# Kernel optimization log

Measured on AMD Instinct MI355X. Metric: run time of the kernel, lower is better.

The kernel has to match this reference:

```python
import jax, jax.numpy as jnp
import numpy as np

NUM_GROUPS = 32
EPS = 1e-5


def setup_inputs() -> dict:
    key = jax.random.key(0)
    ks = jax.random.split(key, 6)
    B, C, H, W = 8, 128, 64, 64
    d = C // 8
    x = jax.random.normal(ks[0], (B, C, H, W), dtype=jnp.float32)
    # conv 1x1 weights stored as [out_ch, in_ch]; scaled like torch kaiming-uniform-ish
    s = 1.0 / np.sqrt(C)
    return {
        "x": x,
        "gn_w": jnp.ones((C,), jnp.float32),
        "gn_b": jnp.zeros((C,), jnp.float32),
        "q_w": jax.random.normal(ks[1], (d, C), jnp.float32) * s,
        "q_b": jnp.zeros((d,), jnp.float32),
        "k_w": jax.random.normal(ks[2], (d, C), jnp.float32) * s,
        "k_b": jnp.zeros((d,), jnp.float32),
        "v_w": jax.random.normal(ks[3], (C, C), jnp.float32) * s,
        "v_b": jnp.zeros((C,), jnp.float32),
        "p_w": jax.random.normal(ks[4], (C, C), jnp.float32) * s,
        "p_b": jnp.zeros((C,), jnp.float32),
    }


def _group_norm(x, w, b):
    B, C, H, W = x.shape
    g = NUM_GROUPS
    xr = x.reshape(B, g, C // g, H, W)
    mu = xr.mean(axis=(2, 3, 4), keepdims=True)
    var = xr.var(axis=(2, 3, 4), keepdims=True)
    xn = ((xr - mu) * jax.lax.rsqrt(var + EPS)).reshape(B, C, H, W)
    return xn * w[None, :, None, None] + b[None, :, None, None]


def reference(x, gn_w, gn_b, q_w, q_b, k_w, k_b, v_w, v_b, p_w, p_b):
    B, C, H, W = x.shape
    N = H * W
    h_ = _group_norm(x, gn_w, gn_b)            # [B,C,H,W]
    hf = h_.reshape(B, C, N)                   # flatten spatial
    # 1x1 convs == channel matmuls
    q = jnp.einsum('dc,bcn->bnd', q_w, hf) + q_b[None, None, :]   # [B,N,d]
    k = jnp.einsum('dc,bcn->bnd', k_w, hf) + k_b[None, None, :]   # [B,N,d]
    v = jnp.einsum('ec,bcn->ben', v_w, hf) + v_b[None, :, None]   # [B,C,N]
    d = q.shape[-1]
    scale = jnp.asarray(int(d) ** (-0.5), x.dtype)
    attn = jnp.einsum('bid,bjd->bij', q, k) * scale               # [B,N,N]
    attn = jax.nn.softmax(attn, axis=-1)
    a = jnp.einsum('bcj,bij->bci', v, attn)                       # [B,C,N]
    proj = jnp.einsum('ec,bcn->ben', p_w, a) + p_b[None, :, None]
    return x + proj.reshape(B, C, H, W)
```

## Files before the change

kernel.cpp:

```cpp
#include <hip/hip_runtime.h>
#include <math.h>


typedef short v8s __attribute__((ext_vector_type(8)));
typedef float v16f __attribute__((ext_vector_type(16)));

__device__ __forceinline__ unsigned short f2bf_rne(float f) {
  unsigned u = __float_as_uint(f);
  u += 0x7fffu + ((u >> 16) & 1u);
  return (unsigned short)(u >> 16);
}

__device__ __forceinline__ v8s mk8(unsigned a, unsigned b, unsigned c, unsigned d) {
  union { unsigned u[4]; v8s s; } x;
  x.u[0] = a; x.u[1] = b; x.u[2] = c; x.u[3] = d;
  return x.s;
}

__device__ __forceinline__ unsigned pack_trunc(float hi, float lo) {
  return __builtin_amdgcn_perm(__float_as_uint(hi), __float_as_uint(lo), 0x07060302u);
}

#define VT(b, n, c) (((((size_t)(b) * 256 + ((n) >> 4)) << 7) + (c)) * 16 + ((n) & 15))

#define WSB_MURS   0u
#define WSB_WCATB  4096u
#define WSB_BCAT   49152u
#define WSB_PWB    65536u
#define WSB_QBF    131072u
#define WSB_KBF    1310720u
#define WSB_VBF    2621440u

__global__ __launch_bounds__(512)
void gnprep_kernel(const float* __restrict__ x, float* __restrict__ mu_rs,
                   const float* __restrict__ qw, const float* __restrict__ qb,
                   const float* __restrict__ kw, const float* __restrict__ kb,
                   const float* __restrict__ vw, const float* __restrict__ vb,
                   const float* __restrict__ pw,
                   unsigned short* __restrict__ wcatb, float* __restrict__ bcat,
                   unsigned short* __restrict__ pwb) {
  const int id = blockIdx.x;
  {
    const float qs = 0.36067376022224085f;
    int idx = id * 512 + threadIdx.x;
    if (idx < 160 * 128) {
      int o = idx >> 7, c = idx & 127;
      float val;
      if (o < 16)       val = qw[o * 128 + c] * qs;
      else if (o < 32)  val = kw[(o - 16) * 128 + c];
      else              val = vw[(o - 32) * 128 + c];
      wcatb[idx] = f2bf_rne(val);
    } else if (idx < 160 * 128 + 160) {
      int o = idx - 160 * 128;
      bcat[o] = (o < 16) ? qb[o] * qs : (o < 32) ? kb[o - 16] : vb[o - 32];
    } else if (idx < 160 * 128 + 160 + 128 * 128) {
      int j = idx - (160 * 128 + 160);
      pwb[j] = f2bf_rne(pw[j]);
    }
  }
  const int bg = (id & 7) * 32 + (id >> 3);
  const float4* xp = (const float4*)(x + (size_t)bg * 16384);
  float s = 0.f, ss = 0.f;
#pragma unroll
  for (int u = 0; u < 8; ++u) {
    int i = threadIdx.x + u * 512;
    float4 v = xp[i];
    s  += v.x + v.y + v.z + v.w;
    ss += v.x * v.x + v.y * v.y + v.z * v.z + v.w * v.w;
  }
  for (int off = 32; off > 0; off >>= 1) {
    s  += __shfl_down(s, off, 64);
    ss += __shfl_down(ss, off, 64);
  }
  __shared__ float red[16];
  int lane = threadIdx.x & 63, wid = threadIdx.x >> 6;
  if (lane == 0) { red[wid * 2] = s; red[wid * 2 + 1] = ss; }
  __syncthreads();
  if (threadIdx.x == 0) {
    float S = 0.f, SS = 0.f;
    for (int w = 0; w < 8; ++w) { S += red[w * 2]; SS += red[w * 2 + 1]; }
    float mu  = S * (1.0f / 16384.0f);
    float var = SS * (1.0f / 16384.0f) - mu * mu;
    float rs  = rsqrtf(var + 1e-5f);
    mu_rs[bg * 2]     = mu;
    mu_rs[bg * 2 + 1] = rs;
  }
}

#define HS 136

__global__ __launch_bounds__(512)
void qkv_kernel(const float* __restrict__ x, const float* __restrict__ gnw,
                const float* __restrict__ gnb, const float* __restrict__ mu_rs,
                const unsigned short* __restrict__ wcatb, const float* __restrict__ bcat,
                unsigned short* __restrict__ qTb, unsigned short* __restrict__ kbf,
                unsigned short* __restrict__ vbf) {
  __shared__ alignas(16) unsigned short hs[64 * HS];
  __shared__ float scsh[128], shsh[128], bsh[160];
  const int id = blockIdx.x;
  const int b = id & 7, nb = (id >> 3) << 6;
  const int t = threadIdx.x;
  const int w = t >> 6, lane = t & 63, h = lane >> 5, l = lane & 31;
  const int nsub = w & 1, og = w >> 1;

  if (t < 128) {
    float mu = mu_rs[(b * 32 + (t >> 2)) * 2];
    float rs = mu_rs[(b * 32 + (t >> 2)) * 2 + 1];
    float gw = gnw[t], gb = gnb[t];
    scsh[t] = rs * gw; shsh[t] = gb - mu * rs * gw;
  }
  if (t < 160) bsh[t] = bcat[t];
  __syncthreads();

  const int sn = t & 63;
  const int c00 = (t >> 6) * 4;
  const float* xb = x + ((size_t)b * 128 << 12) + nb + sn;
#pragma unroll
  for (int it = 0; it < 4; ++it) {
    const int c0 = c00 + it * 32;
    float f0 = xb[(size_t)(c0)     << 12] * scsh[c0]     + shsh[c0];
    float f1 = xb[(size_t)(c0 + 1) << 12] * scsh[c0 + 1] + shsh[c0 + 1];
    float f2 = xb[(size_t)(c0 + 2) << 12] * scsh[c0 + 2] + shsh[c0 + 2];
    float f3 = xb[(size_t)(c0 + 3) << 12] * scsh[c0 + 3] + shsh[c0 + 3];
    uint2 u;
    u.x = (unsigned)f2bf_rne(f0) | ((unsigned)f2bf_rne(f1) << 16);
    u.y = (unsigned)f2bf_rne(f2) | ((unsigned)f2bf_rne(f3) << 16);
    *(uint2*)(&hs[sn * HS + c0]) = u;
  }
  __syncthreads();

  const int n = nb + nsub * 32 + l;
  const int otbase = (og == 0) ? 0 : og + 1;
  v16f acc[2];
#pragma unroll
  for (int a2 = 0; a2 < 2; ++a2)
#pragma unroll
    for (int r = 0; r < 16; ++r) acc[a2][r] = 0.f;

#pragma unroll
  for (int ks = 0; ks < 8; ++ks) {
    v8s bf = *(const v8s*)(&hs[(nsub * 32 + l) * HS + ks * 16 + 8 * h]);
    {
      v8s af = *(const v8s*)(wcatb + (otbase * 32 + l) * 128 + ks * 16 + 8 * h);
      acc[0] = __builtin_amdgcn_mfma_f32_32x32x16_bf16(af, bf, acc[0], 0, 0, 0);
    }
    if (og == 0) {
      v8s af = *(const v8s*)(wcatb + (32 + l) * 128 + ks * 16 + 8 * h);
      acc[1] = __builtin_amdgcn_mfma_f32_32x32x16_bf16(af, bf, acc[1], 0, 0, 0);
    }
  }

  if (og == 0) {
    const size_t nqk = ((size_t)b * 4096 + n) << 4;
#pragma unroll
    for (int r = 0; r < 16; ++r) {
      int o = 4 * h + (r & 3) + 8 * (r >> 2);
      unsigned short bv = f2bf_rne(acc[0][r] + bsh[o]);
      if (o < 16) qTb[((size_t)(b * 16 + o) << 12) + n] = bv;
      else        kbf[nqk + o - 16] = bv;
    }
#pragma unroll
    for (int r = 0; r < 16; ++r) {
      int o = 32 + 4 * h + (r & 3) + 8 * (r >> 2);
      vbf[VT(b, n, o - 32)] = f2bf_rne(acc[1][r] + bsh[o]);
    }
  } else {
#pragma unroll
    for (int r = 0; r < 16; ++r) {
      int o = otbase * 32 + 4 * h + (r & 3) + 8 * (r >> 2);
      vbf[VT(b, n, o - 32)] = f2bf_rne(acc[0][r] + bsh[o]);
    }
  }
}

#define OTS 136

__global__ __launch_bounds__(256)
void attn_kernel(const unsigned short* __restrict__ qTb,
                 const unsigned short* __restrict__ kbf,
                 const unsigned short* __restrict__ vbf,
                 const unsigned short* __restrict__ pwb,
                 const float* __restrict__ pb,
                 const float* __restrict__ x,
                 float* __restrict__ out) {
  __shared__ alignas(16) float ovs[9216];
  __shared__ float l_lds[64];
  __shared__ float pbs[128];

  const int id = blockIdx.x;
  const int b = id & 7, i0 = (id >> 3) << 6;
  const int t = threadIdx.x;
  const int w = t >> 6, lane = t & 63, h = lane >> 5, l = lane & 31;
  const int jsub = w & 1, ihalf = w >> 1;

  const unsigned short* kg = kbf + ((size_t)b << 16) + jsub * 512 + l * 16 + 8 * h;
  const unsigned short* vg = vbf + ((size_t)b << 19) + jsub * 4096 + l * 16 + 8 * h;

  if (t < 128) pbs[t] = pb[t];
  if (t < 64) l_lds[t] = 0.f;

  const int iglob = i0 + ihalf * 32 + l;
  unsigned qd[4];
#pragma unroll
  for (int e = 0; e < 4; ++e) {
    unsigned lo = qTb[((size_t)(b * 16 + 8 * h + 2 * e) << 12) + iglob];
    unsigned hi = qTb[((size_t)(b * 16 + 8 * h + 2 * e + 1) << 12) + iglob];
    qd[e] = lo | (hi << 16);
  }
  const v8s qf = mk8(qd[0], qd[1], qd[2], qd[3]);

  v16f zc;
#pragma unroll
  for (int r = 0; r < 16; ++r) zc[r] = 0.f;
  v16f acc[4];
#pragma unroll
  for (int ct = 0; ct < 4; ++ct)
#pragma unroll
    for (int r = 0; r < 16; ++r) acc[ct][r] = 0.f;
  float ls = 0.f;

  __syncthreads();

  v8s kf = *(const v8s*)kg;
  v8s vf[8];
#pragma unroll
  for (int ct = 0; ct < 4; ++ct) {
    vf[2 * ct]     = *(const v8s*)(vg + ct * 512);
    vf[2 * ct + 1] = *(const v8s*)(vg + 2048 + ct * 512);
  }

#pragma unroll 2
  for (int tile = 0; tile < 64; ++tile) {
    const int tn = (tile + 1) & 63;

    v8s kn = *(const v8s*)(kg + (size_t)tn * 1024);
    v8s vn[8];
    const unsigned short* vt = vg + (size_t)tn * 8192;
#pragma unroll
    for (int ct = 0; ct < 4; ++ct) {
      vn[2 * ct]     = *(const v8s*)(vt + ct * 512);
      vn[2 * ct + 1] = *(const v8s*)(vt + 2048 + ct * 512);
    }

    v16f st = __builtin_amdgcn_mfma_f32_32x32x16_bf16(kf, qf, zc, 0, 0, 0);
    float pe[16];
#pragma unroll
    for (int r = 0; r < 16; ++r) { pe[r] = __builtin_amdgcn_exp2f(st[r]); ls += pe[r]; }
    unsigned G[8];
#pragma unroll
    for (int g = 0; g < 4; ++g) {
      G[2 * g]     = pack_trunc(pe[4 * g + 1], pe[4 * g]);
      G[2 * g + 1] = pack_trunc(pe[4 * g + 3], pe[4 * g + 2]);
    }
    unsigned S0 = h ? G[0] : G[2], S1 = h ? G[1] : G[3];
    unsigned S2 = h ? G[4] : G[6], S3 = h ? G[5] : G[7];
    unsigned R0 = (unsigned)__shfl_xor((int)S0, 32, 64);
    unsigned R1 = (unsigned)__shfl_xor((int)S1, 32, 64);
    unsigned R2 = (unsigned)__shfl_xor((int)S2, 32, 64);
    unsigned R3 = (unsigned)__shfl_xor((int)S3, 32, 64);
    v8s pf0 = h ? mk8(R0, R1, G[2], G[3]) : mk8(G[0], G[1], R0, R1);
    v8s pf1 = h ? mk8(R2, R3, G[6], G[7]) : mk8(G[4], G[5], R2, R3);

#pragma unroll
    for (int ct = 0; ct < 4; ++ct) {
      acc[ct] = __builtin_amdgcn_mfma_f32_32x32x16_bf16(vf[2 * ct],     pf0, acc[ct], 0, 0, 0);
      acc[ct] = __builtin_amdgcn_mfma_f32_32x32x16_bf16(vf[2 * ct + 1], pf1, acc[ct], 0, 0, 0);
    }

    kf = kn;
#pragma unroll
    for (int u = 0; u < 8; ++u) vf[u] = vn[u];
  }

  atomicAdd(&l_lds[ihalf * 32 + l], ls);
  __syncthreads();

  float* const ov = ovs;
  if (jsub == 1) {
#pragma unroll
    for (int ct = 0; ct < 4; ++ct)
#pragma unroll
      for (int q = 0; q < 4; ++q) {
        float4 v4 = {acc[ct][4 * q], acc[ct][4 * q + 1],
                     acc[ct][4 * q + 2], acc[ct][4 * q + 3]};
        *(float4*)&ov[((ct * 2 + ihalf) * 32 + l) * 36 + 4 * h + 8 * q] = v4;
      }
  }
  __syncthreads();
  if (jsub == 0) {
#pragma unroll
    for (int ct = 0; ct < 4; ++ct)
#pragma unroll
      for (int q = 0; q < 4; ++q) {
        float4 v4 = *(float4*)&ov[((ct * 2 + ihalf) * 32 + l) * 36 + 4 * h + 8 * q];
        acc[ct][4 * q]     += v4.x;
        acc[ct][4 * q + 1] += v4.y;
        acc[ct][4 * q + 2] += v4.z;
        acc[ct][4 * q + 3] += v4.w;
      }
  }
  __syncthreads();

  unsigned short* const oT = (unsigned short*)ovs;
  if (jsub == 0) {
    const float li = 1.f / l_lds[ihalf * 32 + l];
    const int nrow = ihalf * 32 + l;
#pragma unroll
    for (int ct = 0; ct < 4; ++ct)
#pragma unroll
      for (int r = 0; r < 16; r += 2) {
        int c = ct * 32 + 4 * h + (r & 3) + 8 * (r >> 2);
        unsigned dw = (unsigned)f2bf_rne(acc[ct][r] * li) |
                      ((unsigned)f2bf_rne(acc[ct][r + 1] * li) << 16);
        *(unsigned*)(&oT[nrow * OTS + c]) = dw;
      }
  }
  __syncthreads();

#pragma unroll
  for (int nsub = 0; nsub < 2; ++nsub) {
    v16f a2;
#pragma unroll
    for (int r = 0; r < 16; ++r) a2[r] = 0.f;
#pragma unroll
    for (int ks = 0; ks < 8; ++ks) {
      v8s bf = *(const v8s*)(&oT[(nsub * 32 + l) * OTS + ks * 16 + 8 * h]);
      v8s af = *(const v8s*)(pwb + (w * 32 + l) * 128 + ks * 16 + 8 * h);
      a2 = __builtin_amdgcn_mfma_f32_32x32x16_bf16(af, bf, a2, 0, 0, 0);
    }
    const int n = i0 + nsub * 32 + l;
#pragma unroll
    for (int r = 0; r < 16; ++r) {
      int e = w * 32 + 4 * h + (r & 3) + 8 * (r >> 2);
      size_t idx = ((size_t)(b * 128 + e) << 12) + n;
      out[idx] = a2[r] + pbs[e] + x[idx];
    }
  }
}

extern "C" void kernel_launch(void* const* d_in, const int* in_sizes, int n_in,
                              void* d_out, int out_size, void* d_ws, size_t ws_size,
                              hipStream_t stream) {
  const float* x   = (const float*)d_in[0];
  const float* gnw = (const float*)d_in[1];
  const float* gnb = (const float*)d_in[2];
  const float* qw  = (const float*)d_in[3];
  const float* qb  = (const float*)d_in[4];
  const float* kw  = (const float*)d_in[5];
  const float* kb  = (const float*)d_in[6];
  const float* vw  = (const float*)d_in[7];
  const float* vb  = (const float*)d_in[8];
  const float* pw  = (const float*)d_in[9];
  const float* pb  = (const float*)d_in[10];
  float* out = (float*)d_out;
  char* ws = (char*)d_ws;

  float* mu_rs = (float*)(ws + WSB_MURS);
  unsigned short* wcatb = (unsigned short*)(ws + WSB_WCATB);
  float* bcat = (float*)(ws + WSB_BCAT);
  unsigned short* pwb = (unsigned short*)(ws + WSB_PWB);
  unsigned short* qTb = (unsigned short*)(ws + WSB_QBF);
  unsigned short* kbf = (unsigned short*)(ws + WSB_KBF);
  unsigned short* vbf = (unsigned short*)(ws + WSB_VBF);

  hipLaunchKernelGGL(gnprep_kernel, dim3(256), dim3(512), 0, stream,
                     x, mu_rs, qw, qb, kw, kb, vw, vb, pw, wcatb, bcat, pwb);
  hipLaunchKernelGGL(qkv_kernel, dim3(512), dim3(512), 0, stream,
                     x, gnw, gnb, mu_rs, wcatb, bcat, qTb, kbf, vbf);
  hipLaunchKernelGGL(attn_kernel, dim3(512), dim3(256), 0, stream,
                     qTb, kbf, vbf, pwb, pb, x, out);
}
```

Before: 153.2 us.

## Split attention key tiles across two wave groups with 512-thread blocks

Doubles the attention block to 8 waves. The two halves process alternating key tiles, then their accumulators are reduced through LDS in two stages. It also replaces the lane shuffles with v_permlane32_swap, raises MFMA issue priority with s_setprio, splits the row-sum accumulator into four partial sums, and spreads the output projection across all 8 waves. The intent is more latency hiding and more parallelism per block, at the cost of a larger LDS footprint, extra reduction barriers, and possibly fewer resident blocks per CU.

Measured after the change: 158.3 us. 3.4% more time.

```diff
diff --git a/kernel.cpp b/kernel.cpp
--- a/kernel.cpp
+++ b/kernel.cpp
@@ -174,8 +174,9 @@
 }
 
 #define OTS 136
-
-__global__ __launch_bounds__(256)
+#define OVSL 4608
+
+__global__ __launch_bounds__(512)
 void attn_kernel(const unsigned short* __restrict__ qTb,
                  const unsigned short* __restrict__ kbf,
                  const unsigned short* __restrict__ vbf,
@@ -183,7 +184,7 @@
                  const float* __restrict__ pb,
                  const float* __restrict__ x,
                  float* __restrict__ out) {
-  __shared__ alignas(16) float ovs[9216];
+  __shared__ alignas(16) float ovs[4 * OVSL];
   __shared__ float l_lds[64];
   __shared__ float pbs[128];
 
@@ -191,7 +192,7 @@
   const int b = id & 7, i0 = (id >> 3) << 6;
   const int t = threadIdx.x;
   const int w = t >> 6, lane = t & 63, h = lane >> 5, l = lane & 31;
-  const int jsub = w & 1, ihalf = w >> 1;
+  const int jsub = w & 1, ihalf = (w >> 1) & 1, par = w >> 2;
 
   const unsigned short* kg = kbf + ((size_t)b << 16) + jsub * 512 + l * 16 + 8 * h;
   const unsigned short* vg = vbf + ((size_t)b << 19) + jsub * 4096 + l * 16 + 8 * h;
@@ -217,21 +218,24 @@
   for (int ct = 0; ct < 4; ++ct)
 #pragma unroll
     for (int r = 0; r < 16; ++r) acc[ct][r] = 0.f;
-  float ls = 0.f;
-
-  __syncthreads();
-
-  v8s kf = *(const v8s*)kg;
+  float ls0 = 0.f, ls1 = 0.f, ls2 = 0.f, ls3 = 0.f;
+
+  __syncthreads();
+
+  v8s kf = *(const v8s*)(kg + (size_t)par * 1024);
   v8s vf[8];
-#pragma unroll
-  for (int ct = 0; ct < 4; ++ct) {
-    vf[2 * ct]     = *(const v8s*)(vg + ct * 512);
-    vf[2 * ct + 1] = *(const v8s*)(vg + 2048 + ct * 512);
+  {
+    const unsigned short* vp = vg + (size_t)par * 8192;
+#pragma unroll
+    for (int ct = 0; ct < 4; ++ct) {
+      vf[2 * ct]     = *(const v8s*)(vp + ct * 512);
+      vf[2 * ct + 1] = *(const v8s*)(vp + 2048 + ct * 512);
+    }
   }
 
 #pragma unroll 2
-  for (int tile = 0; tile < 64; ++tile) {
-    const int tn = (tile + 1) & 63;
+  for (int tile = par; tile < 64; tile += 2) {
+    const int tn = (tile + 2) & 63;
 
     v8s kn = *(const v8s*)(kg + (size_t)tn * 1024);
     v8s vn[8];
@@ -242,57 +246,66 @@
       vn[2 * ct + 1] = *(const v8s*)(vt + 2048 + ct * 512);
     }
 
+    __builtin_amdgcn_s_setprio(1);
     v16f st = __builtin_amdgcn_mfma_f32_32x32x16_bf16(kf, qf, zc, 0, 0, 0);
+    __builtin_amdgcn_s_setprio(0);
     float pe[16];
 #pragma unroll
-    for (int r = 0; r < 16; ++r) { pe[r] = __builtin_amdgcn_exp2f(st[r]); ls += pe[r]; }
+    for (int r = 0; r < 16; ++r) pe[r] = __builtin_amdgcn_exp2f(st[r]);
+    ls0 += pe[0] + pe[4] + pe[8]  + pe[12];
+    ls1 += pe[1] + pe[5] + pe[9]  + pe[13];
+    ls2 += pe[2] + pe[6] + pe[10] + pe[14];
+    ls3 += pe[3] + pe[7] + pe[11] + pe[15];
     unsigned G[8];
 #pragma unroll
     for (int g = 0; g < 4; ++g) {
       G[2 * g]     = pack_trunc(pe[4 * g + 1], pe[4 * g]);
       G[2 * g + 1] = pack_trunc(pe[4 * g + 3], pe[4 * g + 2]);
     }
-    unsigned S0 = h ? G[0] : G[2], S1 = h ? G[1] : G[3];
-    unsigned S2 = h ? G[4] : G[6], S3 = h ? G[5] : G[7];
-    unsigned R0 = (unsigned)__shfl_xor((int)S0, 32, 64);
-    unsigned R1 = (unsigned)__shfl_xor((int)S1, 32, 64);
-    unsigned R2 = (unsigned)__shfl_xor((int)S2, 32, 64);
-    unsigned R3 = (unsigned)__shfl_xor((int)S3, 32, 64);
-    v8s pf0 = h ? mk8(R0, R1, G[2], G[3]) : mk8(G[0], G[1], R0, R1);
-    v8s pf1 = h ? mk8(R2, R3, G[6], G[7]) : mk8(G[4], G[5], R2, R3);
-
+    unsigned A0 = G[0], B0 = G[2], A1 = G[1], B1 = G[3];
+    unsigned A2 = G[4], B2 = G[6], A3 = G[5], B3 = G[7];
+    asm("v_permlane32_swap_b32 %0, %1" : "+v"(A0), "+v"(B0));
+    asm("v_permlane32_swap_b32 %0, %1" : "+v"(A1), "+v"(B1));
+    asm("v_permlane32_swap_b32 %0, %1" : "+v"(A2), "+v"(B2));
+    asm("v_permlane32_swap_b32 %0, %1" : "+v"(A3), "+v"(B3));
+    v8s pf0 = mk8(A0, A1, B0, B1);
+    v8s pf1 = mk8(A2, A3, B2, B3);
+
+    __builtin_amdgcn_s_setprio(1);
 #pragma unroll
     for (int ct = 0; ct < 4; ++ct) {
       acc[ct] = __builtin_amdgcn_mfma_f32_32x32x16_bf16(vf[2 * ct],     pf0, acc[ct], 0, 0, 0);
       acc[ct] = __builtin_amdgcn_mfma_f32_32x32x16_bf16(vf[2 * ct + 1], pf1, acc[ct], 0, 0, 0);
     }
+    __builtin_amdgcn_s_setprio(0);
 
     kf = kn;
 #pragma unroll
     for (int u = 0; u < 8; ++u) vf[u] = vn[u];
   }
 
-  atomicAdd(&l_lds[ihalf * 32 + l], ls);
-  __syncthreads();
+  atomicAdd(&l_lds[ihalf * 32 + l], (ls0 + ls1) + (ls2 + ls3));
 
   float* const ov = ovs;
-  if (jsub == 1) {
+  if (par == 1) {
+    const int s = (jsub * 2 + ihalf) * OVSL;
 #pragma unroll
     for (int ct = 0; ct < 4; ++ct)
 #pragma unroll
       for (int q = 0; q < 4; ++q) {
         float4 v4 = {acc[ct][4 * q], acc[ct][4 * q + 1],
                      acc[ct][4 * q + 2], acc[ct][4 * q + 3]};
-        *(float4*)&ov[((ct * 2 + ihalf) * 32 + l) * 36 + 4 * h + 8 * q] = v4;
+        *(float4*)&ov[s + (ct * 32 + l) * 36 + 4 * h + 8 * q] = v4;
       }
   }
   __syncthreads();
-  if (jsub == 0) {
+  if (par == 0) {
+    const int s = (jsub * 2 + ihalf) * OVSL;
 #pragma unroll
     for (int ct = 0; ct < 4; ++ct)
 #pragma unroll
       for (int q = 0; q < 4; ++q) {
-        float4 v4 = *(float4*)&ov[((ct * 2 + ihalf) * 32 + l) * 36 + 4 * h + 8 * q];
+        float4 v4 = *(float4*)&ov[s + (ct * 32 + l) * 36 + 4 * h + 8 * q];
         acc[ct][4 * q]     += v4.x;
         acc[ct][4 * q + 1] += v4.y;
         acc[ct][4 * q + 2] += v4.z;
@@ -300,9 +313,35 @@
       }
   }
   __syncthreads();
+  if (par == 0 && jsub == 1) {
+    const int s = ihalf * OVSL;
+#pragma unroll
+    for (int ct = 0; ct < 4; ++ct)
+#pragma unroll
+      for (int q = 0; q < 4; ++q) {
+        float4 v4 = {acc[ct][4 * q], acc[ct][4 * q + 1],
+                     acc[ct][4 * q + 2], acc[ct][4 * q + 3]};
+        *(float4*)&ov[s + (ct * 32 + l) * 36 + 4 * h + 8 * q] = v4;
+      }
+  }
+  __syncthreads();
+  if (par == 0 && jsub == 0) {
+    const int s = ihalf * OVSL;
+#pragma unroll
+    for (int ct = 0; ct < 4; ++ct)
+#pragma unroll
+      for (int q = 0; q < 4; ++q) {
+        float4 v4 = *(float4*)&ov[s + (ct * 32 + l) * 36 + 4 * h + 8 * q];
+        acc[ct][4 * q]     += v4.x;
+        acc[ct][4 * q + 1] += v4.y;
+        acc[ct][4 * q + 2] += v4.z;
+        acc[ct][4 * q + 3] += v4.w;
+      }
+  }
+  __syncthreads();
 
   unsigned short* const oT = (unsigned short*)ovs;
-  if (jsub == 0) {
+  if (par == 0 && jsub == 0) {
     const float li = 1.f / l_lds[ihalf * 32 + l];
     const int nrow = ihalf * 32 + l;
 #pragma unroll
@@ -317,21 +356,21 @@
   }
   __syncthreads();
 
-#pragma unroll
-  for (int nsub = 0; nsub < 2; ++nsub) {
+  {
+    const int eg = w >> 1, nsub = w & 1;
     v16f a2;
 #pragma unroll
     for (int r = 0; r < 16; ++r) a2[r] = 0.f;
 #pragma unroll
     for (int ks = 0; ks < 8; ++ks) {
       v8s bf = *(const v8s*)(&oT[(nsub * 32 + l) * OTS + ks * 16 + 8 * h]);
-      v8s af = *(const v8s*)(pwb + (w * 32 + l) * 128 + ks * 16 + 8 * h);
+      v8s af = *(const v8s*)(pwb + (eg * 32 + l) * 128 + ks * 16 + 8 * h);
       a2 = __builtin_amdgcn_mfma_f32_32x32x16_bf16(af, bf, a2, 0, 0, 0);
     }
     const int n = i0 + nsub * 32 + l;
 #pragma unroll
     for (int r = 0; r < 16; ++r) {
-      int e = w * 32 + 4 * h + (r & 3) + 8 * (r >> 2);
+      int e = eg * 32 + 4 * h + (r & 3) + 8 * (r >> 2);
       size_t idx = ((size_t)(b * 128 + e) << 12) + n;
       out[idx] = a2[r] + pbs[e] + x[idx];
     }
@@ -367,6 +406,6 @@
                      x, mu_rs, qw, qb, kw, kb, vw, vb, pw, wcatb, bcat, pwb);
   hipLaunchKernelGGL(qkv_kernel, dim3(512), dim3(512), 0, stream,
                      x, gnw, gnb, mu_rs, wcatb, bcat, qTb, kbf, vbf);
-  hipLaunchKernelGGL(attn_kernel, dim3(512), dim3(256), 0, stream,
+  hipLaunchKernelGGL(attn_kernel, dim3(512), dim3(512), 0, stream,
                      qTb, kbf, vbf, pwb, pb, x, out);
 }
```

## Stage V tiles through LDS with async global_load_lds double buffering

Applied to the files above, without the earlier changes.

V tiles were loaded by every wave straight into registers and each tile was fetched twice, once per ihalf wave pair. They are now copied asynchronously from global memory into a double-buffered LDS region with global_load_lds, and every wave reads its fragments from LDS. This removes the duplicate global V traffic and the eight-register prefetch buffers, at the cost of a block-wide barrier every tile. It also swaps the shfl_xor exchange for v_permlane32_swap, splits the row-sum accumulator into four chains, and raises wave priority around the MFMA block.

New measurement: 155.2 us. No clear change (+1.3%).

```diff
diff --git a/kernel.cpp b/kernel.cpp
--- a/kernel.cpp
+++ b/kernel.cpp
@@ -19,6 +19,12 @@
 
 __device__ __forceinline__ unsigned pack_trunc(float hi, float lo) {
   return __builtin_amdgcn_perm(__float_as_uint(hi), __float_as_uint(lo), 0x07060302u);
+}
+
+__device__ __forceinline__ void gl_lds16(const void* g, void* l) {
+  __builtin_amdgcn_global_load_lds(
+      (const __attribute__((address_space(1))) unsigned int*)g,
+      (__attribute__((address_space(3))) unsigned int*)l, 16, 0, 0);
 }
 
 #define VT(b, n, c) (((((size_t)(b) * 256 + ((n) >> 4)) << 7) + (c)) * 16 + ((n) & 15))
@@ -183,7 +189,7 @@
                  const float* __restrict__ pb,
                  const float* __restrict__ x,
                  float* __restrict__ out) {
-  __shared__ alignas(16) float ovs[9216];
+  __shared__ alignas(16) unsigned char smem[36864];
   __shared__ float l_lds[64];
   __shared__ float pbs[128];
 
@@ -194,7 +200,7 @@
   const int jsub = w & 1, ihalf = w >> 1;
 
   const unsigned short* kg = kbf + ((size_t)b << 16) + jsub * 512 + l * 16 + 8 * h;
-  const unsigned short* vg = vbf + ((size_t)b << 19) + jsub * 4096 + l * 16 + 8 * h;
+  const unsigned short* vgb = vbf + ((size_t)b << 19);
 
   if (t < 128) pbs[t] = pb[t];
   if (t < 64) l_lds[t] = 0.f;
@@ -217,65 +223,72 @@
   for (int ct = 0; ct < 4; ++ct)
 #pragma unroll
     for (int r = 0; r < 16; ++r) acc[ct][r] = 0.f;
-  float ls = 0.f;
-
-  __syncthreads();
-
+  float ls0 = 0.f, ls1 = 0.f, ls2 = 0.f, ls3 = 0.f;
+
+#pragma unroll
+  for (int qi = 0; qi < 4; ++qi) {
+    const int ch = qi * 4 + w;
+    gl_lds16((const char*)vgb + ch * 1024 + lane * 16,
+             (char*)smem + ch * 1024);
+  }
   v8s kf = *(const v8s*)kg;
-  v8s vf[8];
-#pragma unroll
-  for (int ct = 0; ct < 4; ++ct) {
-    vf[2 * ct]     = *(const v8s*)(vg + ct * 512);
-    vf[2 * ct + 1] = *(const v8s*)(vg + 2048 + ct * 512);
-  }
-
-#pragma unroll 2
+  __syncthreads();
+
   for (int tile = 0; tile < 64; ++tile) {
+    unsigned short* const cur = (unsigned short*)(smem + (size_t)(tile & 1) * 16384);
+    char* const nxt = (char*)smem + (size_t)((tile + 1) & 1) * 16384;
     const int tn = (tile + 1) & 63;
 
+    const char* vt = (const char*)vgb + (size_t)tn * 16384;
+#pragma unroll
+    for (int qi = 0; qi < 4; ++qi) {
+      const int ch = qi * 4 + w;
+      gl_lds16(vt + ch * 1024 + lane * 16, nxt + ch * 1024);
+    }
     v8s kn = *(const v8s*)(kg + (size_t)tn * 1024);
-    v8s vn[8];
-    const unsigned short* vt = vg + (size_t)tn * 8192;
-#pragma unroll
-    for (int ct = 0; ct < 4; ++ct) {
-      vn[2 * ct]     = *(const v8s*)(vt + ct * 512);
-      vn[2 * ct + 1] = *(const v8s*)(vt + 2048 + ct * 512);
-    }
 
     v16f st = __builtin_amdgcn_mfma_f32_32x32x16_bf16(kf, qf, zc, 0, 0, 0);
     float pe[16];
 #pragma unroll
-    for (int r = 0; r < 16; ++r) { pe[r] = __builtin_amdgcn_exp2f(st[r]); ls += pe[r]; }
+    for (int r = 0; r < 16; ++r) pe[r] = __builtin_amdgcn_exp2f(st[r]);
+    ls0 += pe[0] + pe[4] + pe[8]  + pe[12];
+    ls1 += pe[1] + pe[5] + pe[9]  + pe[13];
+    ls2 += pe[2] + pe[6] + pe[10] + pe[14];
+    ls3 += pe[3] + pe[7] + pe[11] + pe[15];
     unsigned G[8];
 #pragma unroll
     for (int g = 0; g < 4; ++g) {
       G[2 * g]     = pack_trunc(pe[4 * g + 1], pe[4 * g]);
       G[2 * g + 1] = pack_trunc(pe[4 * g + 3], pe[4 * g + 2]);
     }
-    unsigned S0 = h ? G[0] : G[2], S1 = h ? G[1] : G[3];
-    unsigned S2 = h ? G[4] : G[6], S3 = h ? G[5] : G[7];
-    unsigned R0 = (unsigned)__shfl_xor((int)S0, 32, 64);
-    unsigned R1 = (unsigned)__shfl_xor((int)S1, 32, 64);
-    unsigned R2 = (unsigned)__shfl_xor((int)S2, 32, 64);
-    unsigned R3 = (unsigned)__shfl_xor((int)S3, 32, 64);
-    v8s pf0 = h ? mk8(R0, R1, G[2], G[3]) : mk8(G[0], G[1], R0, R1);
-    v8s pf1 = h ? mk8(R2, R3, G[6], G[7]) : mk8(G[4], G[5], R2, R3);
-
+    unsigned A0 = G[0], B0 = G[2], A1 = G[1], B1 = G[3];
+    unsigned A2 = G[4], B2 = G[6], A3 = G[5], B3 = G[7];
+    asm("v_permlane32_swap_b32 %0, %1" : "+v"(A0), "+v"(B0));
+    asm("v_permlane32_swap_b32 %0, %1" : "+v"(A1), "+v"(B1));
+    asm("v_permlane32_swap_b32 %0, %1" : "+v"(A2), "+v"(B2));
+    asm("v_permlane32_swap_b32 %0, %1" : "+v"(A3), "+v"(B3));
+    v8s pf0 = mk8(A0, A1, B0, B1);
+    v8s pf1 = mk8(A2, A3, B2, B3);
+
+    const unsigned short* vj = cur + jsub * 4096 + l * 16 + 8 * h;
+    __builtin_amdgcn_s_setprio(1);
 #pragma unroll
     for (int ct = 0; ct < 4; ++ct) {
-      acc[ct] = __builtin_amdgcn_mfma_f32_32x32x16_bf16(vf[2 * ct],     pf0, acc[ct], 0, 0, 0);
-      acc[ct] = __builtin_amdgcn_mfma_f32_32x32x16_bf16(vf[2 * ct + 1], pf1, acc[ct], 0, 0, 0);
-    }
+      v8s vf0 = *(const v8s*)(vj + ct * 512);
+      v8s vf1 = *(const v8s*)(vj + 2048 + ct * 512);
+      acc[ct] = __builtin_amdgcn_mfma_f32_32x32x16_bf16(vf0, pf0, acc[ct], 0, 0, 0);
+      acc[ct] = __builtin_amdgcn_mfma_f32_32x32x16_bf16(vf1, pf1, acc[ct], 0, 0, 0);
+    }
+    __builtin_amdgcn_s_setprio(0);
 
     kf = kn;
-#pragma unroll
-    for (int u = 0; u < 8; ++u) vf[u] = vn[u];
-  }
-
-  atomicAdd(&l_lds[ihalf * 32 + l], ls);
-  __syncthreads();
-
-  float* const ov = ovs;
+    __syncthreads();
+  }
+
+  atomicAdd(&l_lds[ihalf * 32 + l], (ls0 + ls1) + (ls2 + ls3));
+  __syncthreads();
+
+  float* const ov = (float*)smem;
   if (jsub == 1) {
 #pragma unroll
     for (int ct = 0; ct < 4; ++ct)
@@ -301,7 +314,7 @@
   }
   __syncthreads();
 
-  unsigned short* const oT = (unsigned short*)ovs;
+  unsigned short* const oT = (unsigned short*)smem;
   if (jsub == 0) {
     const float li = 1.f / l_lds[ihalf * 32 + l];
     const int nrow = ihalf * 32 + l;
```

## Triple-buffer K/V register prefetch and use permlane32 swap in attention loop

Applied to the files above, without the earlier changes.

Replaces the double-buffered register prefetch of K and V tiles with a three-stage rotation, so each tile's loads are issued two iterations ahead of use. The cross-half P exchange switches from two-sided shuffles to v_permlane32_swap, and the PV MFMAs are bracketed with s_setprio to favour matrix issue. The row-sum accumulation is split into four partial sums to shorten the dependency chain, and launch bounds request one block per CU. The extra buffer raises VGPR pressure and could reduce occupancy or cause spills.

Result: no change. 153.3 us (+0.1%).

```diff
diff --git a/kernel.cpp b/kernel.cpp
--- a/kernel.cpp
+++ b/kernel.cpp
@@ -175,7 +175,49 @@
 
 #define OTS 136
 
-__global__ __launch_bounds__(256)
+#define STAGE(T, VL, KL) {                                        \
+  const int tn_ = ((T) + 2) & 63;                                 \
+  const unsigned short* vt_ = vg + (size_t)tn_ * 8192;            \
+  _Pragma("unroll") for (int ct = 0; ct < 4; ++ct) {              \
+    VL[2 * ct]     = *(const v8s*)(vt_ + ct * 512);               \
+    VL[2 * ct + 1] = *(const v8s*)(vt_ + 2048 + ct * 512);        \
+  }                                                               \
+  KL = *(const v8s*)(kg + (size_t)tn_ * 1024);                    \
+}
+
+#define COMPUTE(VU, KU) {                                                   \
+  v16f st = __builtin_amdgcn_mfma_f32_32x32x16_bf16(KU, qf, zc, 0, 0, 0);   \
+  float pe[16];                                                             \
+  _Pragma("unroll") for (int r = 0; r < 16; ++r)                            \
+    pe[r] = __builtin_amdgcn_exp2f(st[r]);                                  \
+  ls0 += pe[0] + pe[4] + pe[8]  + pe[12];                                   \
+  ls1 += pe[1] + pe[5] + pe[9]  + pe[13];                                   \
+  ls2 += pe[2] + pe[6] + pe[10] + pe[14];                                   \
+  ls3 += pe[3] + pe[7] + pe[11] + pe[15];                                   \
+  unsigned G[8];                                                            \
+  _Pragma("unroll") for (int g = 0; g < 4; ++g) {                           \
+    G[2 * g]     = pack_trunc(pe[4 * g + 1], pe[4 * g]);                    \
+    G[2 * g + 1] = pack_trunc(pe[4 * g + 3], pe[4 * g + 2]);                \
+  }                                                                         \
+  unsigned A0 = G[0], B0 = G[2], A1 = G[1], B1 = G[3];                      \
+  unsigned A2 = G[4], B2 = G[6], A3 = G[5], B3 = G[7];                      \
+  asm("v_permlane32_swap_b32 %0, %1" : "+v"(A0), "+v"(B0));                 \
+  asm("v_permlane32_swap_b32 %0, %1" : "+v"(A1), "+v"(B1));                 \
+  asm("v_permlane32_swap_b32 %0, %1" : "+v"(A2), "+v"(B2));                 \
+  asm("v_permlane32_swap_b32 %0, %1" : "+v"(A3), "+v"(B3));                 \
+  v8s pf0 = mk8(A0, A1, B0, B1);                                            \
+  v8s pf1 = mk8(A2, A3, B2, B3);                                            \
+  __builtin_amdgcn_s_setprio(1);                                            \
+  _Pragma("unroll") for (int ct = 0; ct < 4; ++ct) {                        \
+    acc[ct] = __builtin_amdgcn_mfma_f32_32x32x16_bf16(VU[2 * ct],     pf0,  \
+                                                      acc[ct], 0, 0, 0);    \
+    acc[ct] = __builtin_amdgcn_mfma_f32_32x32x16_bf16(VU[2 * ct + 1], pf1,  \
+                                                      acc[ct], 0, 0, 0);    \
+  }                                                                         \
+  __builtin_amdgcn_s_setprio(0);                                            \
+}
+
+__global__ __launch_bounds__(256, 1)
 void attn_kernel(const unsigned short* __restrict__ qTb,
                  const unsigned short* __restrict__ kbf,
                  const unsigned short* __restrict__ vbf,
@@ -217,62 +259,33 @@
   for (int ct = 0; ct < 4; ++ct)
 #pragma unroll
     for (int r = 0; r < 16; ++r) acc[ct][r] = 0.f;
-  float ls = 0.f;
-
-  __syncthreads();
-
-  v8s kf = *(const v8s*)kg;
-  v8s vf[8];
+  float ls0 = 0.f, ls1 = 0.f, ls2 = 0.f, ls3 = 0.f;
+
+  __syncthreads();
+
+  v8s va[8], vb[8], vc[8], ka, kb, kc;
 #pragma unroll
   for (int ct = 0; ct < 4; ++ct) {
-    vf[2 * ct]     = *(const v8s*)(vg + ct * 512);
-    vf[2 * ct + 1] = *(const v8s*)(vg + 2048 + ct * 512);
-  }
-
-#pragma unroll 2
-  for (int tile = 0; tile < 64; ++tile) {
-    const int tn = (tile + 1) & 63;
-
-    v8s kn = *(const v8s*)(kg + (size_t)tn * 1024);
-    v8s vn[8];
-    const unsigned short* vt = vg + (size_t)tn * 8192;
-#pragma unroll
-    for (int ct = 0; ct < 4; ++ct) {
-      vn[2 * ct]     = *(const v8s*)(vt + ct * 512);
-      vn[2 * ct + 1] = *(const v8s*)(vt + 2048 + ct * 512);
-    }
-
-    v16f st = __builtin_amdgcn_mfma_f32_32x32x16_bf16(kf, qf, zc, 0, 0, 0);
-    float pe[16];
-#pragma unroll
-    for (int r = 0; r < 16; ++r) { pe[r] = __builtin_amdgcn_exp2f(st[r]); ls += pe[r]; }
-    unsigned G[8];
-#pragma unroll
-    for (int g = 0; g < 4; ++g) {
-      G[2 * g]     = pack_trunc(pe[4 * g + 1], pe[4 * g]);
-      G[2 * g + 1] = pack_trunc(pe[4 * g + 3], pe[4 * g + 2]);
-    }
-    unsigned S0 = h ? G[0] : G[2], S1 = h ? G[1] : G[3];
-    unsigned S2 = h ? G[4] : G[6], S3 = h ? G[5] : G[7];
-    unsigned R0 = (unsigned)__shfl_xor((int)S0, 32, 64);
-    unsigned R1 = (unsigned)__shfl_xor((int)S1, 32, 64);
-    unsigned R2 = (unsigned)__shfl_xor((int)S2, 32, 64);
-    unsigned R3 = (unsigned)__shfl_xor((int)S3, 32, 64);
-    v8s pf0 = h ? mk8(R0, R1, G[2], G[3]) : mk8(G[0], G[1], R0, R1);
-    v8s pf1 = h ? mk8(R2, R3, G[6], G[7]) : mk8(G[4], G[5], R2, R3);
-
-#pragma unroll
-    for (int ct = 0; ct < 4; ++ct) {
-      acc[ct] = __builtin_amdgcn_mfma_f32_32x32x16_bf16(vf[2 * ct],     pf0, acc[ct], 0, 0, 0);
-      acc[ct] = __builtin_amdgcn_mfma_f32_32x32x16_bf16(vf[2 * ct + 1], pf1, acc[ct], 0, 0, 0);
-    }
-
-    kf = kn;
-#pragma unroll
-    for (int u = 0; u < 8; ++u) vf[u] = vn[u];
-  }
-
-  atomicAdd(&l_lds[ihalf * 32 + l], ls);
+    va[2 * ct]     = *(const v8s*)(vg + ct * 512);
+    va[2 * ct + 1] = *(const v8s*)(vg + 2048 + ct * 512);
+  }
+#pragma unroll
+  for (int ct = 0; ct < 4; ++ct) {
+    vb[2 * ct]     = *(const v8s*)(vg + 8192 + ct * 512);
+    vb[2 * ct + 1] = *(const v8s*)(vg + 8192 + 2048 + ct * 512);
+  }
+  ka = *(const v8s*)kg;
+  kb = *(const v8s*)(kg + 1024);
+
+  for (int i = 0; i < 21; ++i) {
+    const int t3 = 3 * i;
+    { STAGE(t3,     vc, kc); COMPUTE(va, ka); }
+    { STAGE(t3 + 1, va, ka); COMPUTE(vb, kb); }
+    { STAGE(t3 + 2, vb, kb); COMPUTE(vc, kc); }
+  }
+  { STAGE(63, vc, kc); COMPUTE(va, ka); }
+
+  atomicAdd(&l_lds[ihalf * 32 + l], (ls0 + ls1) + (ls2 + ls3));
   __syncthreads();
 
   float* const ov = ovs;
```
